# Kernel tuning notes

Hardware: AMD Instinct MI355X
Metric: run time of the kernel (lower is better)

## Reference

```python
import jax, jax.numpy as jnp
import numpy as np

B, D_IN, UNITS = 2048, 4096, 4096

def setup_inputs() -> dict:
    key = jax.random.key(0)
    k_x, k_m, k_w, k_b = jax.random.split(key, 4)
    x = jax.random.normal(k_x, (B, D_IN), dtype=jnp.float32)
    mask = jax.random.randint(k_m, (D_IN, UNITS), 0, 2).astype(jnp.float32)
    # glorot_uniform kernel
    limit = np.sqrt(6.0 / (D_IN + UNITS)).astype(np.float32)
    W = jax.random.uniform(k_w, (D_IN, UNITS), dtype=jnp.float32, minval=-limit, maxval=limit)
    b = jnp.zeros((UNITS,), dtype=jnp.float32)
    return {"x": x, "mask": mask, "W": W, "b": b}

def reference(x, mask, W, b):
    # Original: build COO sparse tensor of kernel entries where mask != 0,
    # then (sparse_W^T @ x^T)^T == x @ (W masked by mask != 0). Bias added, no activation.
    W_masked = jnp.where(mask != 0.0, W, jnp.zeros((), dtype=W.dtype))
    return x @ W_masked + b
```

## Files before the change

kernel.cpp:

```cpp
#include <hip/hip_runtime.h>

#define M_DIM 2048
#define K_DIM 4096
#define N_DIM 4096
#define KTILES (K_DIM / 64)

typedef unsigned short u16;
typedef unsigned int u32;
typedef __bf16 bf16x8 __attribute__((ext_vector_type(8)));
typedef float f32x4 __attribute__((ext_vector_type(4)));
typedef float f4 __attribute__((ext_vector_type(4)));
typedef u16 u16x8 __attribute__((ext_vector_type(8)));
typedef u32 u32x4 __attribute__((ext_vector_type(4)));

__device__ __forceinline__ u16 f2bf(float f) {
    unsigned int u = __float_as_uint(f);
    u += 0x7fffu + ((u >> 16) & 1u);
    return (u16)(u >> 16);
}

__device__ __forceinline__ u32 pack2(float lo, float hi) {
    u32 a = __float_as_uint(lo); a += 0x7fffu + ((a >> 16) & 1u);
    u32 b = __float_as_uint(hi); b += 0x7fffu + ((b >> 16) & 1u);
    return (a >> 16) | (b & 0xffff0000u);
}

__device__ __forceinline__ void load16(const void* g, void* l) {
    __builtin_amdgcn_global_load_lds(
        (__attribute__((address_space(1))) const void*)g,
        (__attribute__((address_space(3))) void*)l,
        16, 0, 0);
}

__global__ __launch_bounds__(256) void prep(const float* __restrict__ x,
                                            u16* __restrict__ xb,
                                            const float* __restrict__ W,
                                            const float* __restrict__ Msk,
                                            u16* __restrict__ Bt) {
    const int t = threadIdx.x;
    if (blockIdx.x >= 2048) {
        size_t i = ((size_t)(blockIdx.x - 2048) * 256 + t) * 16;
#pragma unroll
        for (int h = 0; h < 2; ++h) {
            f4 v0 = *(const f4*)(x + i + h * 8);
            f4 v1 = *(const f4*)(x + i + h * 8 + 4);
            u16x8 o;
            o[0] = f2bf(v0[0]); o[1] = f2bf(v0[1]); o[2] = f2bf(v0[2]); o[3] = f2bf(v0[3]);
            o[4] = f2bf(v1[0]); o[5] = f2bf(v1[1]); o[6] = f2bf(v1[2]); o[7] = f2bf(v1[3]);
            *(u16x8*)(xb + i + h * 8) = o;
        }
        return;
    }
    const int n0 = (blockIdx.x & 31) * 128;
    const int k0 = (blockIdx.x >> 5) * 64;
    const int ko = t & 7;
    const int ng = t >> 3;

    const float* Wp = W   + (size_t)(k0 + 8 * ko) * N_DIM + n0 + 4 * ng;
    const float* Mp = Msk + (size_t)(k0 + 8 * ko) * N_DIM + n0 + 4 * ng;

    f4 a[8];
#pragma unroll
    for (int j = 0; j < 8; ++j) {
        f4 wv = *(const f4*)(Wp + (size_t)j * N_DIM);
        f4 mv = *(const f4*)(Mp + (size_t)j * N_DIM);
        a[j][0] = mv[0] != 0.f ? wv[0] : 0.f;
        a[j][1] = mv[1] != 0.f ? wv[1] : 0.f;
        a[j][2] = mv[2] != 0.f ? wv[2] : 0.f;
        a[j][3] = mv[3] != 0.f ? wv[3] : 0.f;
    }

    u16* bp = Bt + (size_t)(n0 + 4 * ng) * K_DIM + k0 + 8 * ko;
#pragma unroll
    for (int i = 0; i < 4; ++i) {
        u32x4 o;
        o[0] = pack2(a[0][i], a[1][i]);
        o[1] = pack2(a[2][i], a[3][i]);
        o[2] = pack2(a[4][i], a[5][i]);
        o[3] = pack2(a[6][i], a[7][i]);
        *(u32x4*)(bp + (size_t)i * K_DIM) = o;
    }
}

__global__ __launch_bounds__(512, 2) void gemm8(const u16* __restrict__ A,
                                                const u16* __restrict__ Bt,
                                                const float* __restrict__ bias,
                                                float* __restrict__ C) {
    __shared__ __align__(16) u16 As[2][128 * 64];
    __shared__ __align__(16) u16 Bs[2][256 * 64];

    const int t  = threadIdx.x;
    const int bn = blockIdx.x;
    const int bm = blockIdx.y;

    const int srow   = t >> 3;
    const int schunk = (t & 7) ^ (srow & 7);
    const u16* gA = A  + (size_t)(bm * 128 + srow) * K_DIM + schunk * 8;
    const u16* gB = Bt + (size_t)(bn * 256 + srow) * K_DIM + schunk * 8;

    const int lane = t & 63;
    const int wv   = t >> 6;
    const int wm = (wv >> 2) * 64;
    const int wn = (wv & 3) * 64;
    const int fr = lane & 15;
    const int q  = lane >> 4;
    const int sw = fr & 7;
    const int col0 = ((0 + q) ^ sw) * 8;
    const int col1 = ((4 + q) ^ sw) * 8;

#define STAGE_A(buf, kt) do { \
    load16(gA + (size_t)(kt) * 64,               (buf) + t * 8); \
    load16(gA + (size_t)(kt) * 64 + 64 * K_DIM,  (buf) + 4096 + t * 8); } while (0)
#define STAGE_B0(buf, kt) do { \
    load16(gB + (size_t)(kt) * 64,               (buf) + t * 8); \
    load16(gB + (size_t)(kt) * 64 + 64 * K_DIM,  (buf) + 4096 + t * 8); } while (0)
#define STAGE_B1(buf, kt) do { \
    load16(gB + (size_t)(kt) * 64 + 128 * K_DIM, (buf) + 8192 + t * 8); \
    load16(gB + (size_t)(kt) * 64 + 192 * K_DIM, (buf) + 12288 + t * 8); } while (0)

#define RD(dst, base, row0) do { \
    dst[0][0] = *(const bf16x8*)((base) + ((row0) + fr) * 64 + col0); \
    dst[0][1] = *(const bf16x8*)((base) + ((row0) + fr) * 64 + col1); \
    dst[1][0] = *(const bf16x8*)((base) + ((row0) + 16 + fr) * 64 + col0); \
    dst[1][1] = *(const bf16x8*)((base) + ((row0) + 16 + fr) * 64 + col1); } while (0)

#define MM(fa, fb, mq, nq) do { \
    __builtin_amdgcn_s_setprio(1); \
    _Pragma("unroll") \
    for (int kx = 0; kx < 2; ++kx) \
      _Pragma("unroll") \
      for (int i2 = 0; i2 < 2; ++i2) \
        _Pragma("unroll") \
        for (int j2 = 0; j2 < 2; ++j2) \
          acc[(mq) * 2 + i2][(nq) * 2 + j2] = __builtin_amdgcn_mfma_f32_16x16x32_bf16( \
              fa[i2][kx], fb[j2][kx], acc[(mq) * 2 + i2][(nq) * 2 + j2], 0, 0, 0); \
    __builtin_amdgcn_s_setprio(0); } while (0)

    f32x4 acc[4][4] = {};

    STAGE_A(As[0], 0);
    STAGE_B0(Bs[0], 0);
    STAGE_B1(Bs[0], 0);

    for (int kt = 0; kt < KTILES; ++kt) {
        const int cur = kt & 1;
        const int nxt = cur ^ 1;
        const int kn  = (kt + 1) & (KTILES - 1);
        const u16* a = As[cur];
        const u16* b = Bs[cur];
        bf16x8 fA0[2][2], fA1[2][2], fB0[2][2], fB1[2][2];

        asm volatile("s_waitcnt vmcnt(2) lgkmcnt(0)" ::: "memory");
        __builtin_amdgcn_s_barrier();
        RD(fA0, a, wm);
        RD(fB0, b, wn);
        STAGE_A(As[nxt], kn);
        MM(fA0, fB0, 0, 0);

        asm volatile("s_waitcnt vmcnt(2) lgkmcnt(0)" ::: "memory");
        __builtin_amdgcn_s_barrier();
        RD(fB1, b, wn + 32);
        STAGE_B0(Bs[nxt], kn);
        MM(fA0, fB1, 0, 1);

        RD(fA1, a, wm + 32);
        STAGE_B1(Bs[nxt], kn);
        MM(fA1, fB1, 1, 1);

        MM(fA1, fB0, 1, 0);
    }

    const int rb = q * 4;
#pragma unroll
    for (int i = 0; i < 4; ++i) {
#pragma unroll
        for (int j = 0; j < 4; ++j) {
            int n = bn * 256 + wn + j * 16 + fr;
            float bv = bias[n];
#pragma unroll
            for (int r = 0; r < 4; ++r) {
                int m = bm * 128 + wm + i * 16 + rb + r;
                C[(size_t)m * N_DIM + n] = acc[i][j][r] + bv;
            }
        }
    }
#undef STAGE_A
#undef STAGE_B0
#undef STAGE_B1
#undef RD
#undef MM
}

extern "C" void kernel_launch(void* const* d_in, const int* in_sizes, int n_in,
                              void* d_out, int out_size, void* d_ws, size_t ws_size,
                              hipStream_t stream) {
    const float* x    = (const float*)d_in[0];
    const float* mask = (const float*)d_in[1];
    const float* W    = (const float*)d_in[2];
    const float* bias = (const float*)d_in[3];
    float* out = (float*)d_out;

    u16* Bt = (u16*)d_ws;
    u16* xb = (u16*)d_ws + (size_t)N_DIM * K_DIM;

    prep<<<4096, 256, 0, stream>>>(x, xb, W, mask, Bt);
    gemm8<<<dim3(N_DIM / 256, M_DIM / 128), 512, 0, stream>>>(xb, Bt, bias, out);
}
```

Before: 265.4 us.

## Triple-buffer LDS tiles to prefetch two K-tiles ahead in bf16 GEMM

The GEMM main loop moves from double to triple buffering in LDS, so global-to-LDS loads run two K-tiles ahead and use a rotating set of buffer pointers. All fragment reads for the first half are issued up front. Barriers and the s_setprio brackets are placed around pairs of MFMA groups, and vmcnt waits happen once per iteration instead of twice. The aim is to hide global-load latency better and cut the number of sync points per tile. The cost is LDS use rising to about 144KB per block, which rules out two blocks per CU, though the grid is small enough that this may not matter.

```diff
diff --git a/kernel.cpp b/kernel.cpp
--- a/kernel.cpp
+++ b/kernel.cpp
@@ -86,8 +86,8 @@
                                                 const u16* __restrict__ Bt,
                                                 const float* __restrict__ bias,
                                                 float* __restrict__ C) {
-    __shared__ __align__(16) u16 As[2][128 * 64];
-    __shared__ __align__(16) u16 Bs[2][256 * 64];
+    __shared__ __align__(16) u16 As[3][128 * 64];
+    __shared__ __align__(16) u16 Bs[3][256 * 64];
 
     const int t  = threadIdx.x;
     const int bn = blockIdx.x;
@@ -108,15 +108,10 @@
     const int col0 = ((0 + q) ^ sw) * 8;
     const int col1 = ((4 + q) ^ sw) * 8;
 
-#define STAGE_A(buf, kt) do { \
-    load16(gA + (size_t)(kt) * 64,               (buf) + t * 8); \
-    load16(gA + (size_t)(kt) * 64 + 64 * K_DIM,  (buf) + 4096 + t * 8); } while (0)
-#define STAGE_B0(buf, kt) do { \
-    load16(gB + (size_t)(kt) * 64,               (buf) + t * 8); \
-    load16(gB + (size_t)(kt) * 64 + 64 * K_DIM,  (buf) + 4096 + t * 8); } while (0)
-#define STAGE_B1(buf, kt) do { \
-    load16(gB + (size_t)(kt) * 64 + 128 * K_DIM, (buf) + 8192 + t * 8); \
-    load16(gB + (size_t)(kt) * 64 + 192 * K_DIM, (buf) + 12288 + t * 8); } while (0)
+#define SA(buf, kt, j) load16(gA + (size_t)(kt) * 64 + (size_t)(j) * 64 * K_DIM, \
+                              (buf) + (j) * 4096 + t * 8)
+#define SB(buf, kt, j) load16(gB + (size_t)(kt) * 64 + (size_t)(j) * 64 * K_DIM, \
+                              (buf) + (j) * 4096 + t * 8)
 
 #define RD(dst, base, row0) do { \
     dst[0][0] = *(const bf16x8*)((base) + ((row0) + fr) * 64 + col0); \
@@ -125,7 +120,6 @@
     dst[1][1] = *(const bf16x8*)((base) + ((row0) + 16 + fr) * 64 + col1); } while (0)
 
 #define MM(fa, fb, mq, nq) do { \
-    __builtin_amdgcn_s_setprio(1); \
     _Pragma("unroll") \
     for (int kx = 0; kx < 2; ++kx) \
       _Pragma("unroll") \
@@ -134,40 +128,50 @@
         for (int j2 = 0; j2 < 2; ++j2) \
           acc[(mq) * 2 + i2][(nq) * 2 + j2] = __builtin_amdgcn_mfma_f32_16x16x32_bf16( \
               fa[i2][kx], fb[j2][kx], acc[(mq) * 2 + i2][(nq) * 2 + j2], 0, 0, 0); \
-    __builtin_amdgcn_s_setprio(0); } while (0)
+    } while (0)
 
     f32x4 acc[4][4] = {};
 
-    STAGE_A(As[0], 0);
-    STAGE_B0(Bs[0], 0);
-    STAGE_B1(Bs[0], 0);
+    u16 *aC = (u16*)As[0], *aN1 = (u16*)As[1], *aN2 = (u16*)As[2];
+    u16 *bC = (u16*)Bs[0], *bN1 = (u16*)Bs[1], *bN2 = (u16*)Bs[2];
+
+    SA(aC, 0, 0);  SA(aC, 0, 1);
+    SB(bC, 0, 0);  SB(bC, 0, 1);  SB(bC, 0, 2);  SB(bC, 0, 3);
+    SA(aN1, 1, 0); SA(aN1, 1, 1);
+    SB(bN1, 1, 0); SB(bN1, 1, 1); SB(bN1, 1, 2); SB(bN1, 1, 3);
+    asm volatile("s_waitcnt vmcnt(6)" ::: "memory");
+    __builtin_amdgcn_s_barrier();
 
     for (int kt = 0; kt < KTILES; ++kt) {
-        const int cur = kt & 1;
-        const int nxt = cur ^ 1;
-        const int kn  = (kt + 1) & (KTILES - 1);
-        const u16* a = As[cur];
-        const u16* b = Bs[cur];
+        const int kn = (kt + 2) & (KTILES - 1);
         bf16x8 fA0[2][2], fA1[2][2], fB0[2][2], fB1[2][2];
 
-        asm volatile("s_waitcnt vmcnt(2) lgkmcnt(0)" ::: "memory");
-        __builtin_amdgcn_s_barrier();
-        RD(fA0, a, wm);
-        RD(fB0, b, wn);
-        STAGE_A(As[nxt], kn);
+        RD(fA0, aC, wm);
+        RD(fB0, bC, wn);
+        RD(fB1, bC, wn + 32);
+        SA(aN2, kn, 0); SA(aN2, kn, 1); SB(bN2, kn, 0);
+        __builtin_amdgcn_s_barrier();
+        asm volatile("s_waitcnt lgkmcnt(0)" ::: "memory");
+        __builtin_amdgcn_s_setprio(1);
         MM(fA0, fB0, 0, 0);
-
-        asm volatile("s_waitcnt vmcnt(2) lgkmcnt(0)" ::: "memory");
-        __builtin_amdgcn_s_barrier();
-        RD(fB1, b, wn + 32);
-        STAGE_B0(Bs[nxt], kn);
         MM(fA0, fB1, 0, 1);
-
-        RD(fA1, a, wm + 32);
-        STAGE_B1(Bs[nxt], kn);
+        __builtin_amdgcn_s_setprio(0);
+        __builtin_amdgcn_s_barrier();
+
+        RD(fA1, aC, wm + 32);
+        SB(bN2, kn, 1); SB(bN2, kn, 2); SB(bN2, kn, 3);
+        __builtin_amdgcn_s_barrier();
+        asm volatile("s_waitcnt lgkmcnt(0)" ::: "memory");
+        __builtin_amdgcn_s_setprio(1);
         MM(fA1, fB1, 1, 1);
-
         MM(fA1, fB0, 1, 0);
+        __builtin_amdgcn_s_setprio(0);
+        asm volatile("s_waitcnt vmcnt(6)" ::: "memory");
+        __builtin_amdgcn_s_barrier();
+
+        u16* tmp;
+        tmp = aC; aC = aN1; aN1 = aN2; aN2 = tmp;
+        tmp = bC; bC = bN1; bN1 = bN2; bN2 = tmp;
     }
 
     const int rb = q * 4;
@@ -184,9 +188,8 @@
             }
         }
     }
-#undef STAGE_A
-#undef STAGE_B0
-#undef STAGE_B1
+#undef SA
+#undef SB
 #undef RD
 #undef MM
 }
```

Measured after the change: 253.8 us. 1.05x faster.
